# Kernel tuning notes

Measured on AMD Instinct MI355X. Metric: run time of the kernel, lower is better.

## Reference

```python
import jax, jax.numpy as jnp
import numpy as np

BATCH = 16384
N_IN = 128
CTX = 128
H = 1024
NB = 8                      # num_bins
OUT_MULT = 3 * NB - 1       # widths + heights + derivatives for RQS
TAIL = 3.0                  # tail_bound
SCALE = float(np.sqrt((H * H) // 2))  # sqrt(prod(hidden_dims)//len(hidden_dims))
MIN_W = 1e-3; MIN_H = 1e-3; MIN_D = 1e-3
DPAD = float(np.log(np.exp(1.0 - MIN_D) - 1.0))  # softplus(DPAD)+MIN_D == 1 at boundaries


def _masks():
    # Standard sequential MADE masks. Input degrees 1..n_in, hidden degrees cycle.
    deg_in = np.arange(1, N_IN + 1)
    deg_h = (np.arange(H) % (N_IN - 1)) + 1
    m0 = deg_h[:, None] >= deg_in[None, :]          # [H, N_IN]
    m1 = deg_h[:, None] >= deg_h[None, :]           # [H, H]
    deg_out = np.repeat(deg_in, OUT_MULT)           # matches view(b, n_in, out_mult)
    m2 = deg_out[:, None] > deg_h[None, :]          # [N_IN*OUT_MULT, H]
    return jnp.asarray(m0), jnp.asarray(m1), jnp.asarray(m2)


def setup_inputs() -> dict:
    key = jax.random.key(0)
    k = jax.random.split(key, 6)
    def rn(kk, shape, fan_in):
        return (jax.random.normal(kk, shape, dtype=jnp.float32) * np.sqrt(1.0 / fan_in)).astype(jnp.float32)
    m0, m1, m2 = _masks()
    return {
        "x": jax.random.normal(k[0], (BATCH, N_IN), dtype=jnp.float32),
        "context": jax.random.normal(k[1], (BATCH, CTX), dtype=jnp.float32),
        "ctx_w": rn(k[2], (H, CTX), CTX),
        "w0": rn(k[3], (H, N_IN), N_IN), "b0": jnp.zeros((H,), jnp.float32),
        "w1": rn(k[4], (H, H), H),       "b1": jnp.zeros((H,), jnp.float32),
        "w2": rn(k[5], (N_IN * OUT_MULT, H), H), "b2": jnp.zeros((N_IN * OUT_MULT,), jnp.float32),
        "mask0": m0, "mask1": m1, "mask2": m2,
    }


def _rqs(x, uw, uh, ud):
    # x: [B, D]; uw, uh: [B, D, NB]; ud: [B, D, NB-1]
    inside = jnp.abs(x) <= TAIL
    xc = jnp.clip(x, -TAIL, TAIL)

    w = MIN_W + (1.0 - MIN_W * NB) * jax.nn.softmax(uw, axis=-1)
    cw = jnp.cumsum(w, axis=-1)
    cw = jnp.concatenate([jnp.zeros_like(cw[..., :1]), cw], axis=-1)
    cw = 2.0 * TAIL * cw - TAIL
    cw = cw.at[..., 0].set(-TAIL).at[..., -1].set(TAIL)
    widths = cw[..., 1:] - cw[..., :-1]

    h = MIN_H + (1.0 - MIN_H * NB) * jax.nn.softmax(uh, axis=-1)
    ch = jnp.cumsum(h, axis=-1)
    ch = jnp.concatenate([jnp.zeros_like(ch[..., :1]), ch], axis=-1)
    ch = 2.0 * TAIL * ch - TAIL
    ch = ch.at[..., 0].set(-TAIL).at[..., -1].set(TAIL)
    heights = ch[..., 1:] - ch[..., :-1]

    pad = jnp.full(ud.shape[:-1] + (1,), DPAD, ud.dtype)
    d = MIN_D + jax.nn.softplus(jnp.concatenate([pad, ud, pad], axis=-1))  # [B, D, NB+1]

    # bucketize: bin index per element (NB is small; comparison-sum beats searchsorted here)
    idx = jnp.clip(jnp.sum((xc[..., None] >= cw).astype(jnp.int32), axis=-1) - 1, 0, NB - 1)
    g = lambda a, i: jnp.take_along_axis(a, i[..., None], axis=-1)[..., 0]

    in_cw = g(cw, idx); in_w = g(widths, idx)
    in_ch = g(ch, idx); in_h = g(heights, idx)
    delta = in_h / in_w
    d0 = g(d, idx); d1 = g(d, idx + 1)

    theta = (xc - in_cw) / in_w
    t1m = theta * (1.0 - theta)
    denom = delta + (d0 + d1 - 2.0 * delta) * t1m
    num = in_h * (delta * theta * theta + d0 * t1m)
    y = in_ch + num / denom
    logdet = (2.0 * jnp.log(delta)
              + jnp.log(d1 * theta * theta + 2.0 * delta * t1m + d0 * (1.0 - theta) ** 2)
              - 2.0 * jnp.log(denom))

    y = jnp.where(inside, y, x)          # identity linear tails
    logdet = jnp.where(inside, logdet, 0.0)
    return y, logdet


def reference(x, context, ctx_w, w0, b0, w1, b1, w2, b2, mask0, mask1, mask2):
    m0 = mask0.astype(w0.dtype); m1 = mask1.astype(w1.dtype); m2 = mask2.astype(w2.dtype)
    hdn = jax.nn.relu(context @ ctx_w.T + x @ (w0 * m0).T + b0)
    hdn = jax.nn.relu(hdn @ (w1 * m1).T + b1)
    out = (hdn @ (w2 * m2).T + b2).reshape(-1, N_IN, OUT_MULT)
    uw = out[..., :NB] / SCALE
    uh = out[..., NB:2 * NB] / SCALE
    ud = out[..., 2 * NB:]
    y, ld = _rqs(x, uw, uh, ud)
    return y, jnp.sum(ld, axis=-1)
```

## Files before the change

kernel.cpp:

```cpp
#include <hip/hip_runtime.h>
#include <cstdint>
#include <cstddef>

#define BATCH   16384
#define N_IN    128
#define CTX     128
#define HDIM    1024
#define NB      8
#define OUT_MULT 23
#define OUT_PAD 24
#define NOUTP   (N_IN * OUT_PAD)
#define KCAT    (CTX + N_IN)

typedef __bf16 bf16x8 __attribute__((ext_vector_type(8)));
typedef float  f32x4  __attribute__((ext_vector_type(4)));

__device__ __forceinline__ uint16_t f2bf(float f) {
    union { float f; uint32_t u; } v; v.f = f;
    uint32_t u = v.u;
    u += 0x7FFFu + ((u >> 16) & 1u);
    return (uint16_t)(u >> 16);
}

__device__ __forceinline__ int kpref_dev(int d) {
    return (d <= 8) ? 9 * d : 72 + 8 * (d - 8);
}
__device__ __forceinline__ int dpos_dev(int p) {
    return (p < 72) ? (p / 9) : (8 + ((p - 72) >> 3));
}
__device__ __forceinline__ int h_of(int p) {
    if (p < 72) { int d = p / 9, j = p - 9 * d; return d + 127 * j; }
    int q = p - 72; int d = 8 + (q >> 3); int j = q & 7; return d + 127 * j;
}

__device__ __forceinline__ void async_ld16(const void* g, const void* l) {
    __builtin_amdgcn_global_load_lds(
        (__attribute__((address_space(1))) void*)(uintptr_t)g,
        (__attribute__((address_space(3))) void*)(uint32_t)(uintptr_t)l,
        16, 0, 0);
}


__global__ void pack_all(
    const float* __restrict__ x,    const float* __restrict__ ctx,
    const float* __restrict__ ctx_w,const float* __restrict__ w0,
    const float* __restrict__ b0,   const float* __restrict__ w1,
    const float* __restrict__ b1,   const float* __restrict__ w2,
    const float* __restrict__ b2,
    uint16_t* __restrict__ xcat, uint16_t* __restrict__ wcat,
    uint16_t* __restrict__ w1m,  uint16_t* __restrict__ w2p,
    float* __restrict__ b0p, float* __restrict__ b1p, float* __restrict__ b2p,
    float* __restrict__ ldz)
{
    __shared__ float srow[HDIM];
    const int blk = blockIdx.x;
    const int tid = threadIdx.x;

    if (blk < 4096) {
        int idx4 = (blk * 256 + tid) * 4;
        int b = idx4 >> 8, c = idx4 & 255;
        f32x4 v = (c < CTX) ? *(const f32x4*)(ctx + (b << 7) + c)
                            : *(const f32x4*)(x   + (b << 7) + (c - CTX));
        ushort4 o;
        o.x = f2bf(v[0]); o.y = f2bf(v[1]); o.z = f2bf(v[2]); o.w = f2bf(v[3]);
        *(ushort4*)(xcat + idx4) = o;
    } else if (blk < 5120) {
        int idx = (blk - 4096) * 256 + tid;
        int p = idx >> 8, c = idx & 255;
        int h = h_of(p);
        float v;
        if (c < CTX) v = ctx_w[(h << 7) + c];
        else {
            int col = c - CTX;
            v = (dpos_dev(p) >= col) ? w0[(h << 7) + col] : 0.0f;
        }
        wcat[idx] = f2bf(v);
    } else if (blk < 6144) {
        const int po = blk - 5120;
        const int drow = dpos_dev(po);
        const float* src = w1 + (size_t)h_of(po) * HDIM;
        *((f32x4*)srow + tid) = *((const f32x4*)src + tid);
        __syncthreads();
        ushort4 o;
#pragma unroll
        for (int e = 0; e < 4; ++e) {
            int pi = 4 * tid + e;
            float v = (drow >= dpos_dev(pi)) ? srow[h_of(pi)] : 0.0f;
            ((uint16_t*)&o)[e] = f2bf(v);
        }
        *((ushort4*)(w1m + (size_t)po * HDIM) + tid) = o;
    } else if (blk < 9216) {
        const int oo = blk - 6144;
        const int g = oo / OUT_PAD, t = oo - g * OUT_PAD;
        const bool live = (t < OUT_MULT);
        if (live) {
            const float* src = w2 + (size_t)(g * OUT_MULT + t) * HDIM;
            *((f32x4*)srow + tid) = *((const f32x4*)src + tid);
        }
        __syncthreads();
        ushort4 o;
#pragma unroll
        for (int e = 0; e < 4; ++e) {
            int pi = 4 * tid + e;
            float v = (live && g > dpos_dev(pi)) ? srow[h_of(pi)] : 0.0f;
            ((uint16_t*)&o)[e] = f2bf(v);
        }
        *((ushort4*)(w2p + (size_t)oo * HDIM) + tid) = o;
    } else if (blk < 9232) {
        int idx = (blk - 9216) * 256 + tid;
        if (idx < HDIM) {
            int h = h_of(idx);
            b0p[idx] = b0[h];
            b1p[idx] = b1[h];
        } else {
            int oo = idx - HDIM;
            int g = oo / OUT_PAD, t = oo - g * OUT_PAD;
            b2p[oo] = (t < OUT_MULT) ? b2[g * OUT_MULT + t] : 0.0f;
        }
    } else {
        int idx = (blk - 9232) * 256 + tid;
        ldz[idx] = 0.0f;
    }
}


template<int MODE>
__device__ __forceinline__ void gemm_bt_body(
    const uint16_t* __restrict__ A,
    const uint16_t* __restrict__ B,
    const float*    __restrict__ bias,
    uint16_t*       __restrict__ C,
    int N, int K, int NT)
{
    __shared__ __align__(16) uint16_t sA[2][128 * 64];
    __shared__ __align__(16) uint16_t sB[2][128 * 64];

    const int GM    = 64;
    const int per   = GM * NT;
    const int id    = blockIdx.x;
    const int grp   = id / per;
    const int rem   = id - grp * per;
    const int mt    = grp * GM + (rem & (GM - 1));
    const int nt    = (NT - 1) - (rem >> 6);
    const int bm    = mt << 7;
    const int bn    = nt << 7;

    int K_eff;
    if (MODE == 0)      { int dmax = dpos_dev(bn + 127); K_eff = 128 + dmax + 1; }
    else                { int dmax = dpos_dev(bn + 127); K_eff = kpref_dev(dmax + 1); }
    K_eff = min(K, (K_eff + 63) & ~63);

    const int tid   = threadIdx.x;
    const int wid   = tid >> 6;
    const int lane  = tid & 63;
    const int wm    = (wid & 1) << 6;
    const int wn    = (wid >> 1) << 6;
    const int lrow  = lane & 15;
    const int lquad = lane >> 4;

    const f32x4 vzero = {0.0f, 0.0f, 0.0f, 0.0f};
    f32x4 acc[4][4];
#pragma unroll
    for (int i = 0; i < 4; ++i)
#pragma unroll
        for (int j = 0; j < 4; ++j) acc[i][j] = vzero;

    int goff[4];
#pragma unroll
    for (int t = 0; t < 4; ++t) {
        int c = t * 256 + tid;
        int row = c >> 3, j = c & 7;
        int oct = j ^ (row & 7);
        goff[t] = row * K * 2 + oct * 16;
    }
    const char* gA = (const char*)(A + (size_t)bm * K);
    const char* gB = (const char*)(B + (size_t)bn * K);

    const int octx = lrow & 7;

    auto stage = [&](int b, int k0) {
        const int kb = k0 * 2;
#pragma unroll
        for (int t = 0; t < 4; ++t) {
            const int ldsoff = (t * 256 + (wid << 6)) * 16;
            async_ld16(gA + goff[t] + kb, (const char*)sA[b] + ldsoff);
            async_ld16(gB + goff[t] + kb, (const char*)sB[b] + ldsoff);
        }
    };

    stage(0, 0);
    __syncthreads();

    int cur = 0;
    for (int k0 = 0; k0 < K_eff; k0 += 64) {
        if (k0 + 64 < K_eff) stage(cur ^ 1, k0 + 64);

        const uint16_t* rA = sA[cur] + (wm + lrow) * 64;
        const uint16_t* rB = sB[cur] + (wn + lrow) * 64;
#pragma unroll
        for (int ks = 0; ks < 2; ++ks) {
            const int oct = ((ks << 2) | lquad) ^ octx;
            bf16x8 af[4], bfr[4];
#pragma unroll
            for (int i = 0; i < 4; ++i) af[i]  = *(const bf16x8*)(rA + i * 1024 + oct * 8);
#pragma unroll
            for (int j = 0; j < 4; ++j) bfr[j] = *(const bf16x8*)(rB + j * 1024 + oct * 8);
#pragma unroll
            for (int i = 0; i < 4; ++i)
#pragma unroll
                for (int j = 0; j < 4; ++j)
                    acc[i][j] = __builtin_amdgcn_mfma_f32_16x16x32_bf16(
                                    af[i], bfr[j], acc[i][j], 0, 0, 0);
        }

        __syncthreads();
        cur ^= 1;
    }

#pragma unroll
    for (int j = 0; j < 4; ++j) {
        const int col = bn + wn + j * 16 + lrow;
        const float bv = bias[col];
#pragma unroll
        for (int i = 0; i < 4; ++i) {
            const int row0 = bm + wm + i * 16 + (lquad << 2);
#pragma unroll
            for (int r = 0; r < 4; ++r) {
                float v = fmaxf(acc[i][j][r] + bv, 0.0f);
                C[(size_t)(row0 + r) * N + col] = f2bf(v);
            }
        }
    }
}

__global__ __launch_bounds__(256, 2) void gemm1_k(
    const uint16_t* __restrict__ A, const uint16_t* __restrict__ B,
    const float* __restrict__ bias, uint16_t* __restrict__ C,
    int N, int K, int NT)
{ gemm_bt_body<0>(A, B, bias, C, N, K, NT); }

__global__ __launch_bounds__(256, 2) void gemm2_k(
    const uint16_t* __restrict__ A, const uint16_t* __restrict__ B,
    const float* __restrict__ bias, uint16_t* __restrict__ C,
    int N, int K, int NT)
{ gemm_bt_body<1>(A, B, bias, C, N, K, NT); }


__device__ __forceinline__ float frcp(float v) { return __builtin_amdgcn_rcpf(v); }
__device__ __forceinline__ float softplusf(float v) {
    return fmaxf(v, 0.0f) + __logf(1.0f + __expf(-fabsf(v)));
}

__device__ __forceinline__ void spline_eval(const float* __restrict__ pp,
                                            float xv, float& yout, float& ldout)
{
    float p[OUT_PAD];
#pragma unroll
    for (int k = 0; k < OUT_PAD / 4; ++k)
        *(f32x4*)(p + 4 * k) = *(const f32x4*)(pp + 4 * k);

    const float TAILF = 3.0f;
    const float MIN_W = 0.001f, MIN_H = 0.001f, MIN_D = 0.001f;
    const float INV_SCALE = 1.0f / 724.0773439350246f;

    const float xc = fminf(fmaxf(xv, -TAILF), TAILF);

    float uw[NB], uh[NB];
#pragma unroll
    for (int k = 0; k < NB; ++k) { uw[k] = p[k] * INV_SCALE; uh[k] = p[NB + k] * INV_SCALE; }
    float mw = uw[0], mh = uh[0];
#pragma unroll
    for (int k = 1; k < NB; ++k) { mw = fmaxf(mw, uw[k]); mh = fmaxf(mh, uh[k]); }
    float ew[NB], eh[NB], sw = 0.0f, sh = 0.0f;
#pragma unroll
    for (int k = 0; k < NB; ++k) {
        ew[k] = __expf(uw[k] - mw); sw += ew[k];
        eh[k] = __expf(uh[k] - mh); sh += eh[k];
    }
    const float FACW = (1.0f - MIN_W * NB) * frcp(sw);
    const float FACH = (1.0f - MIN_H * NB) * frcp(sh);

    float cw[NB + 1], ch[NB + 1];
    cw[0] = -TAILF; ch[0] = -TAILF;
    float aw = 0.0f, ah = 0.0f;
#pragma unroll
    for (int k = 0; k < NB; ++k) {
        aw += MIN_W + FACW * ew[k];
        ah += MIN_H + FACH * eh[k];
        cw[k + 1] = (k == NB - 1) ? TAILF : 2.0f * TAILF * aw - TAILF;
        ch[k + 1] = (k == NB - 1) ? TAILF : 2.0f * TAILF * ah - TAILF;
    }

    float dd[NB + 1];
    dd[0]  = 1.0f;
    dd[NB] = 1.0f;
#pragma unroll
    for (int k = 1; k < NB; ++k) dd[k] = MIN_D + softplusf(p[2 * NB + (k - 1)]);

    float in_cw = cw[0], cw_n = cw[1], in_ch = ch[0], ch_n = ch[1];
    float d0 = dd[0], d1 = dd[1];
#pragma unroll
    for (int k = 1; k < NB; ++k) {
        const bool ge = (xc >= cw[k]);
        in_cw = ge ? cw[k]     : in_cw;
        cw_n  = ge ? cw[k + 1] : cw_n;
        in_ch = ge ? ch[k]     : in_ch;
        ch_n  = ge ? ch[k + 1] : ch_n;
        d0    = ge ? dd[k]     : d0;
        d1    = ge ? dd[k + 1] : d1;
    }
    const float in_w  = cw_n - in_cw;
    const float in_h  = ch_n - in_ch;
    const float inv_w = frcp(in_w);
    const float delta = in_h * inv_w;
    const float theta = (xc - in_cw) * inv_w;
    const float omt   = 1.0f - theta;
    const float t1m   = theta * omt;
    const float denom = delta + (d0 + d1 - 2.0f * delta) * t1m;
    const float num   = in_h * (delta * theta * theta + d0 * t1m);
    float yv = in_ch + num * frcp(denom);
    float ld = 2.0f * __logf(delta)
             + __logf(d1 * theta * theta + 2.0f * delta * t1m + d0 * omt * omt)
             - 2.0f * __logf(denom);
    const bool inside = fabsf(xv) <= TAILF;
    yout  = inside ? yv : xv;
    ldout = inside ? ld : 0.0f;
}


__global__ __launch_bounds__(256, 2) void gemm3_spline(
    const uint16_t* __restrict__ A,
    const uint16_t* __restrict__ B,
    const float*    __restrict__ bias,
    const float*    __restrict__ x,
    float* __restrict__ y,
    float* __restrict__ ldsum)
{
    __shared__ __align__(16) char smem[40960];
    uint16_t* sA = (uint16_t*)smem;
    uint16_t* sB = (uint16_t*)(smem + 16384);
    float* ep    = (float*)smem;

    const int NT  = 16;
    const int per = 64 * NT;
    const int id  = blockIdx.x;
    const int grp = id / per;
    const int rem = id - grp * per;
    const int mt  = grp * 64 + (rem & 63);
    const int nt  = (NT - 1) - (rem >> 6);
    const int bm  = mt << 7;
    const int bn  = nt * 192;

    const int K = HDIM;
    int K_eff = kpref_dev(8 * nt + 7);
    K_eff = min(K, (K_eff + 63) & ~63);

    const int tid   = threadIdx.x;
    const int wid   = tid >> 6;
    const int lane  = tid & 63;
    const int wm    = (wid & 1) << 6;
    const int wn    = (wid >> 1) * 96;
    const int lrow  = lane & 15;
    const int lquad = lane >> 4;

    const f32x4 vzero = {0.0f, 0.0f, 0.0f, 0.0f};
    f32x4 acc[4][6];
#pragma unroll
    for (int i = 0; i < 4; ++i)
#pragma unroll
        for (int j = 0; j < 6; ++j) acc[i][j] = vzero;

    int goffA[4], goffB[6];
#pragma unroll
    for (int t = 0; t < 4; ++t) {
        int c = t * 256 + tid;
        int row = c >> 3, j = c & 7;
        goffA[t] = row * K * 2 + (j ^ (row & 7)) * 16;
    }
#pragma unroll
    for (int t = 0; t < 6; ++t) {
        int c = t * 256 + tid;
        int row = c >> 3, j = c & 7;
        goffB[t] = row * K * 2 + (j ^ (row & 7)) * 16;
    }
    const char* gA = (const char*)(A + (size_t)bm * K);
    const char* gB = (const char*)(B + (size_t)bn * K);

    const int octx = lrow & 7;
    const uint16_t* rA = sA + (wm + lrow) * 64;
    const uint16_t* rB = sB + (wn + lrow) * 64;

    for (int k0 = 0; k0 < K_eff; k0 += 64) {
        __syncthreads();
        const int kb = k0 * 2;
#pragma unroll
        for (int t = 0; t < 6; ++t) {
            const int ldsoff = (t * 256 + (wid << 6)) * 16;
            if (t < 4)
                async_ld16(gA + goffA[t] + kb, (const char*)sA + ldsoff);
            async_ld16(gB + goffB[t] + kb, (const char*)sB + ldsoff);
        }
        __syncthreads();

#pragma unroll
        for (int ks = 0; ks < 2; ++ks) {
            const int oct = ((ks << 2) | lquad) ^ octx;
            bf16x8 af[4], bfr[6];
#pragma unroll
            for (int i = 0; i < 4; ++i) af[i]  = *(const bf16x8*)(rA + i * 1024 + oct * 8);
#pragma unroll
            for (int j = 0; j < 6; ++j) bfr[j] = *(const bf16x8*)(rB + j * 1024 + oct * 8);
#pragma unroll
            for (int i = 0; i < 4; ++i)
#pragma unroll
                for (int j = 0; j < 6; ++j)
                    acc[i][j] = __builtin_amdgcn_mfma_f32_16x16x32_bf16(
                                    af[i], bfr[j], acc[i][j], 0, 0, 0);
        }
    }

    __syncthreads();

#pragma unroll
    for (int ph = 0; ph < 4; ++ph) {
        if ((wid & 1) == (ph >> 1)) {
#pragma unroll
            for (int ii = 0; ii < 2; ++ii) {
                const int i  = ((ph & 1) << 1) + ii;
                const int l0 = (ii << 4) + (lquad << 2);
#pragma unroll
                for (int j = 0; j < 6; ++j) {
                    const int col = wn + j * 16 + lrow;
                    const float bv = bias[bn + col];
#pragma unroll
                    for (int r = 0; r < 4; ++r)
                        ep[(l0 + r) * 196 + col] = acc[i][j][r] + bv;
                }
            }
        }
        __syncthreads();

        {
            const int row  = tid >> 3;
            const int sg   = tid & 7;
            const int grow = bm + (ph << 5) + row;
            const float xv = x[(size_t)grow * N_IN + (8 * nt + sg)];
            float yv, ld;
            spline_eval(ep + row * 196 + sg * OUT_PAD, xv, yv, ld);
            y[(size_t)grow * N_IN + 8 * nt + sg] = yv;

            ld += __shfl_xor(ld, 1, 64);
            ld += __shfl_xor(ld, 2, 64);
            ld += __shfl_xor(ld, 4, 64);
            if (sg == 0) atomicAdd(&ldsum[grow], ld);
        }
        if (ph < 3) __syncthreads();
    }
}


extern "C" void kernel_launch(void* const* d_in, const int* in_sizes, int n_in,
                              void* d_out, int out_size, void* d_ws, size_t ws_size,
                              hipStream_t stream)
{
    const float* x     = (const float*)d_in[0];
    const float* ctx   = (const float*)d_in[1];
    const float* ctx_w = (const float*)d_in[2];
    const float* w0    = (const float*)d_in[3];
    const float* b0    = (const float*)d_in[4];
    const float* w1    = (const float*)d_in[5];
    const float* b1    = (const float*)d_in[6];
    const float* w2    = (const float*)d_in[7];
    const float* b2    = (const float*)d_in[8];

    char* ws = (char*)d_ws;
    const size_t XCAT_B = (size_t)BATCH * KCAT * 2;
    const size_t H_B    = (size_t)BATCH * HDIM * 2;
    const size_t WCAT_B = (size_t)HDIM * KCAT * 2;
    const size_t W1_B   = (size_t)HDIM * HDIM * 2;
    const size_t W2P_B  = (size_t)NOUTP * HDIM * 2;

    uint16_t* xcat = (uint16_t*)(ws);
    uint16_t* h1   = (uint16_t*)(ws + XCAT_B);
    uint16_t* h2   = (uint16_t*)(ws + XCAT_B + H_B);
    uint16_t* wcat = (uint16_t*)(ws + XCAT_B + 2 * H_B);
    uint16_t* w1m  = (uint16_t*)(ws + XCAT_B + 2 * H_B + WCAT_B);
    uint16_t* w2p  = (uint16_t*)(ws + XCAT_B + 2 * H_B + WCAT_B + W1_B);
    float*    b0p  = (float*)   (ws + XCAT_B + 2 * H_B + WCAT_B + W1_B + W2P_B);
    float*    b1p  = b0p + HDIM;
    float*    b2p  = b1p + HDIM;

    float* yout  = (float*)d_out;
    float* ldout = yout + (size_t)BATCH * N_IN;

    pack_all<<<9296, 256, 0, stream>>>(x, ctx, ctx_w, w0, b0, w1, b1, w2, b2,
                                       xcat, wcat, w1m, w2p, b0p, b1p, b2p,
                                       ldout);

    const dim3 blk(256);
    gemm1_k<<<dim3(128 * (HDIM / 128)), blk, 0, stream>>>(
        xcat, wcat, b0p, h1, HDIM, KCAT, HDIM / 128);
    gemm2_k<<<dim3(128 * (HDIM / 128)), blk, 0, stream>>>(
        h1, w1m, b1p, h2, HDIM, HDIM, HDIM / 128);
    gemm3_spline<<<dim3(128 * 16), blk, 0, stream>>>(
        h2, w2p, b2p, x, yout, ldout);
}
```

Before: 223.0 us.

## Double-buffer gemm3 LDS and use partial vmcnt waits for async loads

```diff
diff --git a/kernel.cpp b/kernel.cpp
--- a/kernel.cpp
+++ b/kernel.cpp
@@ -189,11 +189,16 @@
     };
 
     stage(0, 0);
-    __syncthreads();
 
     int cur = 0;
     for (int k0 = 0; k0 < K_eff; k0 += 64) {
-        if (k0 + 64 < K_eff) stage(cur ^ 1, k0 + 64);
+        if (k0 + 64 < K_eff) {
+            stage(cur ^ 1, k0 + 64);
+            asm volatile("s_waitcnt vmcnt(8)" ::: "memory");
+        } else {
+            asm volatile("s_waitcnt vmcnt(0)" ::: "memory");
+        }
+        __builtin_amdgcn_s_barrier();
 
         const uint16_t* rA = sA[cur] + (wm + lrow) * 64;
         const uint16_t* rB = sB[cur] + (wn + lrow) * 64;
@@ -213,7 +218,7 @@
                                     af[i], bfr[j], acc[i][j], 0, 0, 0);
         }
 
-        __syncthreads();
+        __builtin_amdgcn_s_barrier();
         cur ^= 1;
     }
 
@@ -336,10 +341,8 @@
     float* __restrict__ y,
     float* __restrict__ ldsum)
 {
-    __shared__ __align__(16) char smem[40960];
-    uint16_t* sA = (uint16_t*)smem;
-    uint16_t* sB = (uint16_t*)(smem + 16384);
-    float* ep    = (float*)smem;
+    __shared__ __align__(16) char smem[81920];
+    float* ep = (float*)smem;
 
     const int NT  = 16;
     const int per = 64 * NT;
@@ -387,21 +390,36 @@
     const char* gB = (const char*)(B + (size_t)bn * K);
 
     const int octx = lrow & 7;
-    const uint16_t* rA = sA + (wm + lrow) * 64;
-    const uint16_t* rB = sB + (wn + lrow) * 64;
-
-    for (int k0 = 0; k0 < K_eff; k0 += 64) {
-        __syncthreads();
+
+    auto stage = [&](int b, int k0) {
         const int kb = k0 * 2;
+        char* dA = smem + b * 16384;
+        char* dB = smem + 32768 + b * 24576;
 #pragma unroll
         for (int t = 0; t < 6; ++t) {
             const int ldsoff = (t * 256 + (wid << 6)) * 16;
             if (t < 4)
-                async_ld16(gA + goffA[t] + kb, (const char*)sA + ldsoff);
-            async_ld16(gB + goffB[t] + kb, (const char*)sB + ldsoff);
-        }
-        __syncthreads();
-
+                async_ld16(gA + goffA[t] + kb, dA + ldsoff);
+            async_ld16(gB + goffB[t] + kb, dB + ldsoff);
+        }
+    };
+
+    stage(0, 0);
+
+    int cur = 0;
+    for (int k0 = 0; k0 < K_eff; k0 += 64) {
+        if (k0 + 64 < K_eff) {
+            stage(cur ^ 1, k0 + 64);
+            asm volatile("s_waitcnt vmcnt(10)" ::: "memory");
+        } else {
+            asm volatile("s_waitcnt vmcnt(0)" ::: "memory");
+        }
+        __builtin_amdgcn_s_barrier();
+
+        const uint16_t* rA = (const uint16_t*)(smem + cur * 16384)
+                             + (wm + lrow) * 64;
+        const uint16_t* rB = (const uint16_t*)(smem + 32768 + cur * 24576)
+                             + (wn + lrow) * 64;
 #pragma unroll
         for (int ks = 0; ks < 2; ++ks) {
             const int oct = ((ks << 2) | lquad) ^ octx;
@@ -417,6 +435,9 @@
                     acc[i][j] = __builtin_amdgcn_mfma_f32_16x16x32_bf16(
                                     af[i], bfr[j], acc[i][j], 0, 0, 0);
         }
+
+        __builtin_amdgcn_s_barrier();
+        cur ^= 1;
     }
 
     __syncthreads();
```

Result: faster. 216.8 us (-2.8%).

## Widen hidden-layer GEMM tiles to 128x256 and drop LDS double buffering

Applied to the files above, without the earlier changes.

```diff
diff --git a/kernel.cpp b/kernel.cpp
--- a/kernel.cpp
+++ b/kernel.cpp
@@ -132,8 +132,8 @@
     uint16_t*       __restrict__ C,
     int N, int K, int NT)
 {
-    __shared__ __align__(16) uint16_t sA[2][128 * 64];
-    __shared__ __align__(16) uint16_t sB[2][128 * 64];
+    __shared__ __align__(16) uint16_t sA[128 * 64];
+    __shared__ __align__(16) uint16_t sB[256 * 64];
 
     const int GM    = 64;
     const int per   = GM * NT;
@@ -143,82 +143,79 @@
     const int mt    = grp * GM + (rem & (GM - 1));
     const int nt    = (NT - 1) - (rem >> 6);
     const int bm    = mt << 7;
-    const int bn    = nt << 7;
+    const int bn    = nt << 8;
 
     int K_eff;
-    if (MODE == 0)      { int dmax = dpos_dev(bn + 127); K_eff = 128 + dmax + 1; }
-    else                { int dmax = dpos_dev(bn + 127); K_eff = kpref_dev(dmax + 1); }
+    if (MODE == 0)      { int dmax = dpos_dev(bn + 255); K_eff = 128 + dmax + 1; }
+    else                { int dmax = dpos_dev(bn + 255); K_eff = kpref_dev(dmax + 1); }
     K_eff = min(K, (K_eff + 63) & ~63);
 
     const int tid   = threadIdx.x;
     const int wid   = tid >> 6;
     const int lane  = tid & 63;
     const int wm    = (wid & 1) << 6;
-    const int wn    = (wid >> 1) << 6;
+    const int wn    = (wid >> 1) << 7;
     const int lrow  = lane & 15;
     const int lquad = lane >> 4;
 
     const f32x4 vzero = {0.0f, 0.0f, 0.0f, 0.0f};
-    f32x4 acc[4][4];
+    f32x4 acc[4][8];
 #pragma unroll
     for (int i = 0; i < 4; ++i)
 #pragma unroll
-        for (int j = 0; j < 4; ++j) acc[i][j] = vzero;
-
-    int goff[4];
+        for (int j = 0; j < 8; ++j) acc[i][j] = vzero;
+
+    int goffA[4], goffB[8];
 #pragma unroll
     for (int t = 0; t < 4; ++t) {
         int c = t * 256 + tid;
         int row = c >> 3, j = c & 7;
-        int oct = j ^ (row & 7);
-        goff[t] = row * K * 2 + oct * 16;
+        goffA[t] = row * K * 2 + (j ^ (row & 7)) * 16;
+    }
+#pragma unroll
+    for (int t = 0; t < 8; ++t) {
+        int c = t * 256 + tid;
+        int row = c >> 3, j = c & 7;
+        goffB[t] = row * K * 2 + (j ^ (row & 7)) * 16;
     }
     const char* gA = (const char*)(A + (size_t)bm * K);
     const char* gB = (const char*)(B + (size_t)bn * K);
 
     const int octx = lrow & 7;
-
-    auto stage = [&](int b, int k0) {
+    const uint16_t* rA = sA + (wm + lrow) * 64;
+    const uint16_t* rB = sB + (wn + lrow) * 64;
+
+    for (int k0 = 0; k0 < K_eff; k0 += 64) {
+        __syncthreads();
         const int kb = k0 * 2;
 #pragma unroll
-        for (int t = 0; t < 4; ++t) {
+        for (int t = 0; t < 8; ++t) {
             const int ldsoff = (t * 256 + (wid << 6)) * 16;
-            async_ld16(gA + goff[t] + kb, (const char*)sA[b] + ldsoff);
-            async_ld16(gB + goff[t] + kb, (const char*)sB[b] + ldsoff);
-        }
-    };
-
-    stage(0, 0);
-    __syncthreads();
-
-    int cur = 0;
-    for (int k0 = 0; k0 < K_eff; k0 += 64) {
-        if (k0 + 64 < K_eff) stage(cur ^ 1, k0 + 64);
-
-        const uint16_t* rA = sA[cur] + (wm + lrow) * 64;
-        const uint16_t* rB = sB[cur] + (wn + lrow) * 64;
+            if (t < 4)
+                async_ld16(gA + goffA[t] + kb, (const char*)sA + ldsoff);
+            async_ld16(gB + goffB[t] + kb, (const char*)sB + ldsoff);
+        }
+        __syncthreads();
+
 #pragma unroll
         for (int ks = 0; ks < 2; ++ks) {
             const int oct = ((ks << 2) | lquad) ^ octx;
-            bf16x8 af[4], bfr[4];
+            bf16x8 af[4], bfr[8];
 #pragma unroll
             for (int i = 0; i < 4; ++i) af[i]  = *(const bf16x8*)(rA + i * 1024 + oct * 8);
 #pragma unroll
-            for (int j = 0; j < 4; ++j) bfr[j] = *(const bf16x8*)(rB + j * 1024 + oct * 8);
+            for (int j = 0; j < 8; ++j) bfr[j] = *(const bf16x8*)(rB + j * 1024 + oct * 8);
 #pragma unroll
             for (int i = 0; i < 4; ++i)
 #pragma unroll
-                for (int j = 0; j < 4; ++j)
+                for (int j = 0; j < 8; ++j)
                     acc[i][j] = __builtin_amdgcn_mfma_f32_16x16x32_bf16(
                                     af[i], bfr[j], acc[i][j], 0, 0, 0);
         }
-
-        __syncthreads();
-        cur ^= 1;
-    }
-
-#pragma unroll
-    for (int j = 0; j < 4; ++j) {
+    }
+
+#pragma unroll
+    for (int j = 0; j < 8; ++j) {
         const int col = bn + wn + j * 16 + lrow;
         const float bv = bias[col];
 #pragma unroll
@@ -498,10 +495,10 @@
                                        ldout);
 
     const dim3 blk(256);
-    gemm1_k<<<dim3(128 * (HDIM / 128)), blk, 0, stream>>>(
-        xcat, wcat, b0p, h1, HDIM, KCAT, HDIM / 128);
-    gemm2_k<<<dim3(128 * (HDIM / 128)), blk, 0, stream>>>(
-        h1, w1m, b1p, h2, HDIM, HDIM, HDIM / 128);
+    gemm1_k<<<dim3(128 * (HDIM / 256)), blk, 0, stream>>>(
+        xcat, wcat, b0p, h1, HDIM, KCAT, HDIM / 256);
+    gemm2_k<<<dim3(128 * (HDIM / 256)), blk, 0, stream>>>(
+        h1, w1m, b1p, h2, HDIM, HDIM, HDIM / 256);
     gemm3_spline<<<dim3(128 * 16), blk, 0, stream>>>(
         h2, w2p, b2p, x, yout, ldout);
 }
```

New measurement: 219.2 us. No clear change (-1.7%).
